# Kernel tuning notes

Hardware: AMD Instinct MI355X
Metric: run time of the kernel (lower is better)

## Reference

```python
import jax, jax.numpy as jnp
import numpy as np

N_NODES = 100000
N_EDGES = 1600000
IN_CH = 64
OUT_CH = 32
HEADS = 4
NEG_SLOPE = 0.2


def setup_inputs() -> dict:
    key = jax.random.key(0)
    k = jax.random.split(key, 6)
    x = jax.random.normal(k[0], (N_NODES, IN_CH), dtype=jnp.float32)
    edge_index = jax.random.randint(k[1], (2, N_EDGES), 0, N_NODES, dtype=jnp.int32)
    W = jax.random.normal(k[2], (IN_CH, HEADS * OUT_CH), dtype=jnp.float32) * 0.1
    att_src = jax.random.normal(k[3], (1, HEADS, OUT_CH), dtype=jnp.float32) * 0.1
    att_dst = jax.random.normal(k[4], (1, HEADS, OUT_CH), dtype=jnp.float32) * 0.1
    bias = jnp.zeros((HEADS * OUT_CH,), dtype=jnp.float32)
    return {"x": x, "edge_index": edge_index, "W": W,
            "att_src": att_src, "att_dst": att_dst, "bias": bias}


def reference(x, edge_index, W, att_src, att_dst, bias):
    N = x.shape[0]
    H, C = att_src.shape[1], att_src.shape[2]
    # GATConv defaults: add self loops
    loop = jnp.arange(N, dtype=edge_index.dtype)
    src = jnp.concatenate([edge_index[0], loop])  # [E+N]
    dst = jnp.concatenate([edge_index[1], loop])  # [E+N]
    # linear transform -> [N, H, C]
    h = (x @ W).reshape(N, H, C)
    # per-node attention halves: [N, H]
    a_src = jnp.sum(h * att_src, axis=-1)
    a_dst = jnp.sum(h * att_dst, axis=-1)
    # edge scores with LeakyReLU: [E+N, H]
    e = jax.nn.leaky_relu(a_src[src] + a_dst[dst], negative_slope=NEG_SLOPE)
    # segment softmax over destination nodes (numerically stable)
    m = jax.ops.segment_max(e, dst, num_segments=N)           # [N, H]
    m = jnp.where(jnp.isfinite(m), m, 0.0)
    ex = jnp.exp(e - m[dst])                                   # [E+N, H]
    denom = jax.ops.segment_sum(ex, dst, num_segments=N)      # [N, H]
    alpha = ex / (denom[dst] + 1e-16)                          # [E+N, H]
    # scatter-aggregate weighted source features -> [N, H, C]
    out = jax.ops.segment_sum(h[src] * alpha[:, :, None], dst, num_segments=N)
    out = out.reshape(N, H * C) + bias
    return jax.nn.log_softmax(out, axis=1)
```

## Files before the change

### kernel.cpp

```cpp
#include <hip/hip_runtime.h>
#include <hip/hip_bf16.h>

#define IN_CH 64
#define HC 128
#define NHEAD 4
#define NEG 0.2f
#define CAPB 32
#define BWID 128
#define NB 782
#define CAP2 2560
#define CH1 4096
#define VPT 8

typedef short s16x8 __attribute__((ext_vector_type(8)));
typedef float f32x4 __attribute__((ext_vector_type(4)));

__device__ __forceinline__ float leaky(float v) { return fmaxf(v, NEG * v); }
__device__ __forceinline__ unsigned short f2bf(float f) {
    unsigned int u = __float_as_uint(f);
    u += 0x7fff + ((u >> 16) & 1);
    return (unsigned short)(u >> 16);
}
__device__ __forceinline__ float4 add4(float4 a, float4 b) {
    return make_float4(a.x + b.x, a.y + b.y, a.z + b.z, a.w + b.w);
}
__device__ __forceinline__ float4 leaky4(float4 v) {
    return make_float4(leaky(v.x), leaky(v.y), leaky(v.z), leaky(v.w));
}
__device__ __forceinline__ float4 exp4(float4 v) {
    return make_float4(__expf(v.x), __expf(v.y), __expf(v.z), __expf(v.w));
}
__device__ __forceinline__ float comp4(float4 v, int i) {
    float r = v.x;
    r = (i == 1) ? v.y : r;
    r = (i == 2) ? v.z : r;
    r = (i == 3) ? v.w : r;
    return r;
}

#define ACC8(al, hv)                                                  \
    do {                                                              \
        acc[0] = fmaf((al), __uint_as_float((hv).x << 16), acc[0]);   \
        acc[1] = fmaf((al), __uint_as_float((hv).x & 0xffff0000u), acc[1]); \
        acc[2] = fmaf((al), __uint_as_float((hv).y << 16), acc[2]);   \
        acc[3] = fmaf((al), __uint_as_float((hv).y & 0xffff0000u), acc[3]); \
        acc[4] = fmaf((al), __uint_as_float((hv).z << 16), acc[4]);   \
        acc[5] = fmaf((al), __uint_as_float((hv).z & 0xffff0000u), acc[5]); \
        acc[6] = fmaf((al), __uint_as_float((hv).w << 16), acc[6]);   \
        acc[7] = fmaf((al), __uint_as_float((hv).w & 0xffff0000u), acc[7]); \
    } while (0)

__global__ void __launch_bounds__(512, 4) k_front(
        const float* __restrict__ x, const float* __restrict__ W,
        const float* __restrict__ att_src, const float* __restrict__ att_dst,
        unsigned short* __restrict__ h_bf, float* __restrict__ a_src,
        float* __restrict__ a_dst,
        const int* __restrict__ src, const int* __restrict__ dst,
        int* __restrict__ bcnt, int* __restrict__ pairs,
        int E, int N, int NXB) {
    __shared__ union {
        struct { unsigned short xs[128][72]; unsigned short wt[144][72]; } xf;
        struct { int hist[NB]; int scanbuf[1024]; int startb[NB]; int gbase[NB];
                 int lbuf[CH1]; int gposb[CH1]; } bn;
    } sm;
    const int t = threadIdx.x;
    const int r3 = blockIdx.x % 3;

    if (r3 < 2) {
        const int xb = (blockIdx.x / 3) * 2 + r3;
        if (xb >= NXB) return;
        const int rowbase_blk = xb * 128;

        for (int idx = t; idx < (IN_CH * HC) / 4; idx += 512) {
            const float4 v = ((const float4*)W)[idx];
            const int k = idx >> 5;
            const int c0 = (idx & 31) * 4;
            sm.xf.wt[c0 + 0][k] = f2bf(v.x);
            sm.xf.wt[c0 + 1][k] = f2bf(v.y);
            sm.xf.wt[c0 + 2][k] = f2bf(v.z);
            sm.xf.wt[c0 + 3][k] = f2bf(v.w);
        }
        for (int idx = t; idx < 16 * 64; idx += 512) {
            const int j = idx >> 6, k = idx & 63;
            float v = 0.f;
            if (j < 8) {
                const int h = j & 3;
                const float* att = (j < 4) ? att_src : att_dst;
#pragma unroll
                for (int c = 0; c < 32; ++c)
                    v += W[k * HC + h * 32 + c] * att[h * 32 + c];
            }
            sm.xf.wt[128 + j][k] = f2bf(v);
        }
        for (int idx = t; idx < (128 * IN_CH) / 4; idx += 512) {
            const int row = idx >> 4;
            const int c0 = (idx & 15) * 4;
            const int grow = min(rowbase_blk + row, N - 1);
            const float4 v = ((const float4*)(x + (size_t)grow * IN_CH))[idx & 15];
            const unsigned int p0 = (unsigned int)f2bf(v.x) | ((unsigned int)f2bf(v.y) << 16);
            const unsigned int p1 = (unsigned int)f2bf(v.z) | ((unsigned int)f2bf(v.w) << 16);
            *(uint2*)&sm.xf.xs[row][c0] = make_uint2(p0, p1);
        }
        __syncthreads();

        const int lane = t & 63;
        const int w = t >> 6;
        const int rbase = w * 16;
        const int lr = lane & 15, lq = lane >> 4;

        f32x4 acc[9];
#pragma unroll
        for (int n = 0; n < 9; ++n) acc[n] = (f32x4){0.f, 0.f, 0.f, 0.f};

#pragma unroll
        for (int ks = 0; ks < 2; ++ks) {
            const s16x8 a0 = *(const s16x8*)&sm.xf.xs[rbase + lr][ks * 32 + lq * 8];
#pragma unroll
            for (int n = 0; n < 9; ++n) {
                const s16x8 b = *(const s16x8*)&sm.xf.wt[n * 16 + lr][ks * 32 + lq * 8];
                acc[n] = __builtin_amdgcn_mfma_f32_16x16x32_bf16(a0, b, acc[n], 0, 0, 0);
            }
        }

#pragma unroll
        for (int j = 0; j < 4; ++j) {
            const int grow = rowbase_blk + rbase + lq * 4 + j;
            if (grow >= N) continue;
#pragma unroll
            for (int n = 0; n < 8; ++n)
                h_bf[(size_t)grow * HC + n * 16 + lr] = f2bf(acc[n][j]);
            const float av = acc[8][j];
            if (lr < 4) a_src[grow * NHEAD + lr] = av;
            else if (lr < 8) a_dst[grow * NHEAD + (lr - 4)] = av;
        }
    } else {
        const int bb = blockIdx.x / 3;
        const int base = bb * CH1;
        const int cnt = min(CH1, E - base);

        for (int i = t; i < NB; i += 512) sm.bn.hist[i] = 0;
        __syncthreads();

        int pk[VPT]; int rb[VPT];
#pragma unroll
        for (int k = 0; k < VPT; ++k) {
            const int idx = base + k * 512 + t;
            if (idx < E) {
                const int s = src[idx], d = dst[idx];
                const int b = d >> 7;
                const int dl = d & 127;
                pk[k] = (dl << 17) | s;
                const int rank = atomicAdd(&sm.bn.hist[b], 1);
                rb[k] = (b << 16) | rank;
            } else {
                pk[k] = 0; rb[k] = -1;
            }
        }
        __syncthreads();

        sm.bn.scanbuf[t] = (t < NB) ? sm.bn.hist[t] : 0;
        sm.bn.scanbuf[t + 512] = (t + 512 < NB) ? sm.bn.hist[t + 512] : 0;
        __syncthreads();
        for (int off = 1; off < 1024; off <<= 1) {
            const int a0 = (t >= off) ? sm.bn.scanbuf[t - off] : 0;
            const int a1 = (t + 512 >= off) ? sm.bn.scanbuf[t + 512 - off] : 0;
            __syncthreads();
            sm.bn.scanbuf[t] += a0;
            sm.bn.scanbuf[t + 512] += a1;
            __syncthreads();
        }
        for (int i = t; i < NB; i += 512) {
            const int h = sm.bn.hist[i];
            sm.bn.startb[i] = sm.bn.scanbuf[i] - h;
            sm.bn.gbase[i] = (h > 0) ? atomicAdd(&bcnt[i * 16], h) : 0;
        }
        __syncthreads();

#pragma unroll
        for (int k = 0; k < VPT; ++k) {
            if (rb[k] >= 0) {
                const int b = rb[k] >> 16;
                const int rank = rb[k] & 0xffff;
                const int lpos = sm.bn.startb[b] + rank;
                const int gp = sm.bn.gbase[b] + rank;
                sm.bn.lbuf[lpos] = pk[k];
                sm.bn.gposb[lpos] = (gp < CAP2) ? (b * CAP2 + gp) : -1;
            }
        }
        __syncthreads();

        for (int i = t; i < cnt; i += 512) {
            const int g = sm.bn.gposb[i];
            if (g >= 0) pairs[g] = sm.bn.lbuf[i];
        }
    }
}

__global__ void __launch_bounds__(256) k_fill(
        const int* __restrict__ bcnt, const int* __restrict__ pairs,
        int* __restrict__ srcbuf, int* __restrict__ rowstart,
        int* __restrict__ deg, int N) {
    const int b = blockIdx.x;
    const int t = threadIdx.x;
    __shared__ int scnt[BWID];
    __shared__ int cur[BWID];
    __shared__ int scan2[256];
    __shared__ int slist[CAP2];
    __shared__ int sbase_s;

    int part = 0;
    for (int i = t; i < b; i += 256) part += min(bcnt[i * 16], CAP2);
    scan2[t] = part; __syncthreads();
    for (int off = 128; off > 0; off >>= 1) {
        if (t < off) scan2[t] += scan2[t + off];
        __syncthreads();
    }
    if (t == 0) sbase_s = scan2[0];
    if (t < BWID) scnt[t] = 0;
    __syncthreads();

    const int mc = min(bcnt[b * 16], CAP2);
    const int pb = b * CAP2;

    for (int i = t; i < mc; i += 256)
        atomicAdd(&scnt[pairs[pb + i] >> 17], 1);
    __syncthreads();

    if (t < BWID) scan2[t] = scnt[t];
    __syncthreads();
    for (int off = 1; off < BWID; off <<= 1) {
        const int add = (t >= off && t < BWID) ? scan2[t - off] : 0;
        __syncthreads();
        if (t < BWID) scan2[t] += add;
        __syncthreads();
    }
    if (t < BWID) {
        const int ex = scan2[t] - scnt[t];
        cur[t] = ex;
        const int n = b * BWID + t;
        if (n < N) {
            rowstart[n] = sbase_s + ex;
            deg[n] = scnt[t];
        }
    }
    __syncthreads();

    for (int i = t; i < mc; i += 256) {
        const int e = pairs[pb + i];
        const int p = atomicAdd(&cur[e >> 17], 1);
        slist[p] = e & 0x1ffff;
    }
    __syncthreads();

    for (int i = t; i < mc; i += 256) srcbuf[sbase_s + i] = slist[i];
}

__global__ void __launch_bounds__(256) k_node(
        const int* __restrict__ deg_, const int* __restrict__ rowstart,
        const int* __restrict__ srcbuf,
        const float* __restrict__ a_src, const float* __restrict__ a_dst,
        const unsigned short* __restrict__ h_bf, const float* __restrict__ bias,
        float* __restrict__ out, int N) {
    const int slot = threadIdx.x >> 4;
    const int l = threadIdx.x & 15;
    int n = blockIdx.x * 16 + slot;
    n = min(n, N - 1);
    const int deg = deg_[n];
    const int start = rowstart[n];
    const int dcap = min(deg, CAPB);

    __shared__ float s_ex[16][CAPB + 1][NHEAD];
    __shared__ int   s_src[16][CAPB + 1];

    const float4 ad4  = *(const float4*)(a_dst + n * NHEAD);
    const float4 asn4 = *(const float4*)(a_src + n * NHEAD);

    float4 sum4 = make_float4(0.f, 0.f, 0.f, 0.f);
    for (int j = l; j < dcap; j += 16) {
        const int s = srcbuf[start + j];
        s_src[slot][j] = s;
        const float4 a = *(const float4*)(a_src + s * NHEAD);
        const float4 e4 = exp4(leaky4(add4(a, ad4)));
        *(float4*)&s_ex[slot][j][0] = e4;
        sum4 = add4(sum4, e4);
    }
    for (int j = CAPB + l; j < deg; j += 16) {
        const int s = srcbuf[start + j];
        const float4 a = *(const float4*)(a_src + s * NHEAD);
        sum4 = add4(sum4, exp4(leaky4(add4(a, ad4))));
    }
#pragma unroll
    for (int off = 1; off < 16; off <<= 1) {
        sum4.x += __shfl_xor(sum4.x, off, 64);
        sum4.y += __shfl_xor(sum4.y, off, 64);
        sum4.z += __shfl_xor(sum4.z, off, 64);
        sum4.w += __shfl_xor(sum4.w, off, 64);
    }
    const float4 self4 = exp4(leaky4(add4(asn4, ad4)));
    sum4 = add4(sum4, self4);
    const float4 r4v = make_float4(1.f / (sum4.x + 1e-16f), 1.f / (sum4.y + 1e-16f),
                                   1.f / (sum4.z + 1e-16f), 1.f / (sum4.w + 1e-16f));

    __builtin_amdgcn_wave_barrier();

    const int hd = l >> 2;
    const float rsel = comp4(r4v, hd);
    const float adh  = comp4(ad4, hd);
    float acc[8];
#pragma unroll
    for (int k = 0; k < 8; ++k) acc[k] = 0.f;

    int j = 0;
    for (; j + 2 <= dcap; j += 2) {
        const int s0 = s_src[slot][j];
        const int s1 = s_src[slot][j + 1];
        const uint4 h0 = *(const uint4*)(h_bf + (size_t)s0 * HC + l * 8);
        const uint4 h1 = *(const uint4*)(h_bf + (size_t)s1 * HC + l * 8);
        const float al0 = s_ex[slot][j][hd];
        const float al1 = s_ex[slot][j + 1][hd];
        ACC8(al0, h0);
        ACC8(al1, h1);
    }
    if (j < dcap) {
        const int s0 = s_src[slot][j];
        const uint4 h0 = *(const uint4*)(h_bf + (size_t)s0 * HC + l * 8);
        const float al0 = s_ex[slot][j][hd];
        ACC8(al0, h0);
    }
    for (int jj = CAPB; jj < deg; ++jj) {
        const int s = srcbuf[start + jj];
        const float al = __expf(leaky(a_src[s * NHEAD + hd] + adh));
        const uint4 hv = *(const uint4*)(h_bf + (size_t)s * HC + l * 8);
        ACC8(al, hv);
    }
    {
        const float als = comp4(self4, hd);
        const uint4 hv = *(const uint4*)(h_bf + (size_t)n * HC + l * 8);
        ACC8(als, hv);
    }

    const float4 b0 = *(const float4*)(bias + l * 8);
    const float4 b1 = *(const float4*)(bias + l * 8 + 4);
    acc[0] = acc[0] * rsel + b0.x; acc[1] = acc[1] * rsel + b0.y;
    acc[2] = acc[2] * rsel + b0.z; acc[3] = acc[3] * rsel + b0.w;
    acc[4] = acc[4] * rsel + b1.x; acc[5] = acc[5] * rsel + b1.y;
    acc[6] = acc[6] * rsel + b1.z; acc[7] = acc[7] * rsel + b1.w;

    float mxv = fmaxf(fmaxf(fmaxf(acc[0], acc[1]), fmaxf(acc[2], acc[3])),
                      fmaxf(fmaxf(acc[4], acc[5]), fmaxf(acc[6], acc[7])));
#pragma unroll
    for (int off = 1; off < 16; off <<= 1) mxv = fmaxf(mxv, __shfl_xor(mxv, off, 64));
    float se = 0.f;
#pragma unroll
    for (int k = 0; k < 8; ++k) se += __expf(acc[k] - mxv);
#pragma unroll
    for (int off = 1; off < 16; off <<= 1) se += __shfl_xor(se, off, 64);
    const float lse = mxv + __logf(se);

    float* op = out + (size_t)n * HC + l * 8;
    *(float4*)op = make_float4(acc[0] - lse, acc[1] - lse, acc[2] - lse, acc[3] - lse);
    *(float4*)(op + 4) = make_float4(acc[4] - lse, acc[5] - lse, acc[6] - lse, acc[7] - lse);
}

extern "C" void kernel_launch(void* const* d_in, const int* in_sizes, int n_in,
                              void* d_out, int out_size, void* d_ws, size_t ws_size,
                              hipStream_t stream) {
    const float* x       = (const float*)d_in[0];
    const int*   ei      = (const int*)d_in[1];
    const float* W       = (const float*)d_in[2];
    const float* att_src = (const float*)d_in[3];
    const float* att_dst = (const float*)d_in[4];
    const float* bias    = (const float*)d_in[5];
    float* out = (float*)d_out;

    const int N = in_sizes[0] / IN_CH;
    const int E = in_sizes[1] / 2;
    const int* src = ei;
    const int* dst = ei + E;

    char* wsb = (char*)d_ws;
    unsigned short* h_bf = (unsigned short*)wsb;    wsb += (size_t)N * HC * 2;
    float* a_src  = (float*)wsb;                    wsb += (size_t)N * NHEAD * 4;
    float* a_dst  = (float*)wsb;                    wsb += (size_t)N * NHEAD * 4;
    int*   bcnt   = (int*)wsb;                      wsb += (size_t)NB * 16 * 4;
    int*   pairs  = (int*)wsb;                      wsb += (size_t)NB * CAP2 * 4;
    int*   srcbuf = (int*)wsb;                      wsb += (size_t)E * 4;
    int*   rowstart = (int*)wsb;                    wsb += (size_t)N * 4;
    int*   deg    = (int*)wsb;                      wsb += (size_t)N * 4;

    const int NXB = (N + 127) / 128;
    const int NBB = (E + CH1 - 1) / CH1;

    hipMemsetAsync(bcnt, 0, (size_t)NB * 16 * 4, stream);

    k_front<<<NBB * 3, 512, 0, stream>>>(x, W, att_src, att_dst,
                                         h_bf, a_src, a_dst,
                                         src, dst, bcnt, pairs, E, N, NXB);
    k_fill<<<NB, 256, 0, stream>>>(bcnt, pairs, srcbuf, rowstart, deg, N);
    k_node<<<(N + 15) / 16, 256, 0, stream>>>(deg, rowstart, srcbuf,
                                              a_src, a_dst,
                                              (const unsigned short*)h_bf, bias, out, N);
}
```

Baseline: 211.1 us.

## Fuse bucket CSR fill into node aggregation kernel using shared-memory edge lists

```diff
diff --git a/kernel.cpp b/kernel.cpp
--- a/kernel.cpp
+++ b/kernel.cpp
@@ -50,7 +50,7 @@
         acc[7] = fmaf((al), __uint_as_float((hv).w & 0xffff0000u), acc[7]); \
     } while (0)
 
-__global__ void __launch_bounds__(512, 4) k_front(
+__global__ void __launch_bounds__(512, 2) k_front(
         const float* __restrict__ x, const float* __restrict__ W,
         const float* __restrict__ att_src, const float* __restrict__ att_dst,
         unsigned short* __restrict__ h_bf, float* __restrict__ a_src,
@@ -196,55 +196,41 @@
     }
 }
 
-__global__ void __launch_bounds__(256) k_fill(
+__global__ void __launch_bounds__(256) k_node(
         const int* __restrict__ bcnt, const int* __restrict__ pairs,
-        int* __restrict__ srcbuf, int* __restrict__ rowstart,
-        int* __restrict__ deg, int N) {
+        const float* __restrict__ a_src, const float* __restrict__ a_dst,
+        const unsigned short* __restrict__ h_bf, const float* __restrict__ bias,
+        float* __restrict__ out, int N) {
     const int b = blockIdx.x;
     const int t = threadIdx.x;
-    __shared__ int scnt[BWID];
-    __shared__ int cur[BWID];
-    __shared__ int scan2[256];
-    __shared__ int slist[CAP2];
-    __shared__ int sbase_s;
-
-    int part = 0;
-    for (int i = t; i < b; i += 256) part += min(bcnt[i * 16], CAP2);
-    scan2[t] = part; __syncthreads();
-    for (int off = 128; off > 0; off >>= 1) {
-        if (t < off) scan2[t] += scan2[t + off];
-        __syncthreads();
-    }
-    if (t == 0) sbase_s = scan2[0];
-    if (t < BWID) scnt[t] = 0;
-    __syncthreads();
+    __shared__ int   slist[CAP2];
+    __shared__ int   srow[BWID];
+    __shared__ int   sdeg[BWID];
+    __shared__ int   cur[BWID];
+    __shared__ int   scanb[BWID];
+    __shared__ float s_ex[16][CAPB + 1][NHEAD];
 
     const int mc = min(bcnt[b * 16], CAP2);
     const int pb = b * CAP2;
 
+    if (t < BWID) sdeg[t] = 0;
+    __syncthreads();
     for (int i = t; i < mc; i += 256)
-        atomicAdd(&scnt[pairs[pb + i] >> 17], 1);
-    __syncthreads();
-
-    if (t < BWID) scan2[t] = scnt[t];
+        atomicAdd(&sdeg[pairs[pb + i] >> 17], 1);
+    __syncthreads();
+    if (t < BWID) scanb[t] = sdeg[t];
     __syncthreads();
     for (int off = 1; off < BWID; off <<= 1) {
-        const int add = (t >= off && t < BWID) ? scan2[t - off] : 0;
-        __syncthreads();
-        if (t < BWID) scan2[t] += add;
+        const int add = (t < BWID && t >= off) ? scanb[t - off] : 0;
+        __syncthreads();
+        if (t < BWID) scanb[t] += add;
         __syncthreads();
     }
     if (t < BWID) {
-        const int ex = scan2[t] - scnt[t];
-        cur[t] = ex;
-        const int n = b * BWID + t;
-        if (n < N) {
-            rowstart[n] = sbase_s + ex;
-            deg[n] = scnt[t];
-        }
-    }
-    __syncthreads();
-
+        srow[t] = scanb[t] - sdeg[t];
+        cur[t] = scanb[t] - sdeg[t];
+    }
+    __syncthreads();
     for (int i = t; i < mc; i += 256) {
         const int e = pairs[pb + i];
         const int p = atomicAdd(&cur[e >> 17], 1);
@@ -252,114 +238,113 @@
     }
     __syncthreads();
 
-    for (int i = t; i < mc; i += 256) srcbuf[sbase_s + i] = slist[i];
-}
-
-__global__ void __launch_bounds__(256) k_node(
-        const int* __restrict__ deg_, const int* __restrict__ rowstart,
-        const int* __restrict__ srcbuf,
-        const float* __restrict__ a_src, const float* __restrict__ a_dst,
-        const unsigned short* __restrict__ h_bf, const float* __restrict__ bias,
-        float* __restrict__ out, int N) {
-    const int slot = threadIdx.x >> 4;
-    const int l = threadIdx.x & 15;
-    int n = blockIdx.x * 16 + slot;
-    n = min(n, N - 1);
-    const int deg = deg_[n];
-    const int start = rowstart[n];
-    const int dcap = min(deg, CAPB);
-
-    __shared__ float s_ex[16][CAPB + 1][NHEAD];
-    __shared__ int   s_src[16][CAPB + 1];
-
-    const float4 ad4  = *(const float4*)(a_dst + n * NHEAD);
-    const float4 asn4 = *(const float4*)(a_src + n * NHEAD);
-
-    float4 sum4 = make_float4(0.f, 0.f, 0.f, 0.f);
-    for (int j = l; j < dcap; j += 16) {
-        const int s = srcbuf[start + j];
-        s_src[slot][j] = s;
-        const float4 a = *(const float4*)(a_src + s * NHEAD);
-        const float4 e4 = exp4(leaky4(add4(a, ad4)));
-        *(float4*)&s_ex[slot][j][0] = e4;
-        sum4 = add4(sum4, e4);
-    }
-    for (int j = CAPB + l; j < deg; j += 16) {
-        const int s = srcbuf[start + j];
-        const float4 a = *(const float4*)(a_src + s * NHEAD);
-        sum4 = add4(sum4, exp4(leaky4(add4(a, ad4))));
-    }
-#pragma unroll
-    for (int off = 1; off < 16; off <<= 1) {
-        sum4.x += __shfl_xor(sum4.x, off, 64);
-        sum4.y += __shfl_xor(sum4.y, off, 64);
-        sum4.z += __shfl_xor(sum4.z, off, 64);
-        sum4.w += __shfl_xor(sum4.w, off, 64);
-    }
-    const float4 self4 = exp4(leaky4(add4(asn4, ad4)));
-    sum4 = add4(sum4, self4);
-    const float4 r4v = make_float4(1.f / (sum4.x + 1e-16f), 1.f / (sum4.y + 1e-16f),
-                                   1.f / (sum4.z + 1e-16f), 1.f / (sum4.w + 1e-16f));
-
-    __builtin_amdgcn_wave_barrier();
-
+    const int slot = t >> 4;
+    const int l = t & 15;
     const int hd = l >> 2;
-    const float rsel = comp4(r4v, hd);
-    const float adh  = comp4(ad4, hd);
-    float acc[8];
-#pragma unroll
-    for (int k = 0; k < 8; ++k) acc[k] = 0.f;
-
-    int j = 0;
-    for (; j + 2 <= dcap; j += 2) {
-        const int s0 = s_src[slot][j];
-        const int s1 = s_src[slot][j + 1];
-        const uint4 h0 = *(const uint4*)(h_bf + (size_t)s0 * HC + l * 8);
-        const uint4 h1 = *(const uint4*)(h_bf + (size_t)s1 * HC + l * 8);
-        const float al0 = s_ex[slot][j][hd];
-        const float al1 = s_ex[slot][j + 1][hd];
-        ACC8(al0, h0);
-        ACC8(al1, h1);
-    }
-    if (j < dcap) {
-        const int s0 = s_src[slot][j];
-        const uint4 h0 = *(const uint4*)(h_bf + (size_t)s0 * HC + l * 8);
-        const float al0 = s_ex[slot][j][hd];
-        ACC8(al0, h0);
-    }
-    for (int jj = CAPB; jj < deg; ++jj) {
-        const int s = srcbuf[start + jj];
-        const float al = __expf(leaky(a_src[s * NHEAD + hd] + adh));
-        const uint4 hv = *(const uint4*)(h_bf + (size_t)s * HC + l * 8);
-        ACC8(al, hv);
-    }
-    {
-        const float als = comp4(self4, hd);
-        const uint4 hv = *(const uint4*)(h_bf + (size_t)n * HC + l * 8);
-        ACC8(als, hv);
-    }
-
-    const float4 b0 = *(const float4*)(bias + l * 8);
-    const float4 b1 = *(const float4*)(bias + l * 8 + 4);
-    acc[0] = acc[0] * rsel + b0.x; acc[1] = acc[1] * rsel + b0.y;
-    acc[2] = acc[2] * rsel + b0.z; acc[3] = acc[3] * rsel + b0.w;
-    acc[4] = acc[4] * rsel + b1.x; acc[5] = acc[5] * rsel + b1.y;
-    acc[6] = acc[6] * rsel + b1.z; acc[7] = acc[7] * rsel + b1.w;
-
-    float mxv = fmaxf(fmaxf(fmaxf(acc[0], acc[1]), fmaxf(acc[2], acc[3])),
-                      fmaxf(fmaxf(acc[4], acc[5]), fmaxf(acc[6], acc[7])));
-#pragma unroll
-    for (int off = 1; off < 16; off <<= 1) mxv = fmaxf(mxv, __shfl_xor(mxv, off, 64));
-    float se = 0.f;
-#pragma unroll
-    for (int k = 0; k < 8; ++k) se += __expf(acc[k] - mxv);
-#pragma unroll
-    for (int off = 1; off < 16; off <<= 1) se += __shfl_xor(se, off, 64);
-    const float lse = mxv + __logf(se);
-
-    float* op = out + (size_t)n * HC + l * 8;
-    *(float4*)op = make_float4(acc[0] - lse, acc[1] - lse, acc[2] - lse, acc[3] - lse);
-    *(float4*)(op + 4) = make_float4(acc[4] - lse, acc[5] - lse, acc[6] - lse, acc[7] - lse);
+
+    for (int ng = 0; ng < 8; ++ng) {
+        int dl = ng * 16 + slot;
+        int n = b * BWID + dl;
+        if (n >= N) { n = N - 1; dl = (N - 1) & (BWID - 1); }
+        const int deg = sdeg[dl];
+        const int rs = srow[dl];
+        const int dcap = min(deg, CAPB);
+
+        const float4 ad4  = *(const float4*)(a_dst + n * NHEAD);
+        const float4 asn4 = *(const float4*)(a_src + n * NHEAD);
+
+        float4 sum4 = make_float4(0.f, 0.f, 0.f, 0.f);
+        for (int j = l; j < dcap; j += 16) {
+            const int s = slist[rs + j];
+            const float4 a = *(const float4*)(a_src + s * NHEAD);
+            const float4 e4 = exp4(leaky4(add4(a, ad4)));
+            *(float4*)&s_ex[slot][j][0] = e4;
+            sum4 = add4(sum4, e4);
+        }
+        for (int j = CAPB + l; j < deg; j += 16) {
+            const int s = slist[rs + j];
+            const float4 a = *(const float4*)(a_src + s * NHEAD);
+            sum4 = add4(sum4, exp4(leaky4(add4(a, ad4))));
+        }
+#pragma unroll
+        for (int off = 1; off < 16; off <<= 1) {
+            sum4.x += __shfl_xor(sum4.x, off, 64);
+            sum4.y += __shfl_xor(sum4.y, off, 64);
+            sum4.z += __shfl_xor(sum4.z, off, 64);
+            sum4.w += __shfl_xor(sum4.w, off, 64);
+        }
+        const float4 self4 = exp4(leaky4(add4(asn4, ad4)));
+        sum4 = add4(sum4, self4);
+        const float4 r4v = make_float4(1.f / (sum4.x + 1e-16f), 1.f / (sum4.y + 1e-16f),
+                                       1.f / (sum4.z + 1e-16f), 1.f / (sum4.w + 1e-16f));
+
+        __builtin_amdgcn_wave_barrier();
+
+        const float rsel = comp4(r4v, hd);
+        const float adh  = comp4(ad4, hd);
+        float acc[8];
+#pragma unroll
+        for (int k = 0; k < 8; ++k) acc[k] = 0.f;
+
+        int j = 0;
+        for (; j + 4 <= dcap; j += 4) {
+            const int s0 = slist[rs + j];
+            const int s1 = slist[rs + j + 1];
+            const int s2 = slist[rs + j + 2];
+            const int s3 = slist[rs + j + 3];
+            const uint4 h0 = *(const uint4*)(h_bf + (size_t)s0 * HC + l * 8);
+            const uint4 h1 = *(const uint4*)(h_bf + (size_t)s1 * HC + l * 8);
+            const uint4 h2 = *(const uint4*)(h_bf + (size_t)s2 * HC + l * 8);
+            const uint4 h3 = *(const uint4*)(h_bf + (size_t)s3 * HC + l * 8);
+            const float al0 = s_ex[slot][j][hd];
+            const float al1 = s_ex[slot][j + 1][hd];
+            const float al2 = s_ex[slot][j + 2][hd];
+            const float al3 = s_ex[slot][j + 3][hd];
+            ACC8(al0, h0);
+            ACC8(al1, h1);
+            ACC8(al2, h2);
+            ACC8(al3, h3);
+        }
+        for (; j < dcap; ++j) {
+            const int s0 = slist[rs + j];
+            const uint4 h0 = *(const uint4*)(h_bf + (size_t)s0 * HC + l * 8);
+            const float al0 = s_ex[slot][j][hd];
+            ACC8(al0, h0);
+        }
+        for (int jj = CAPB; jj < deg; ++jj) {
+            const int s = slist[rs + jj];
+            const float al = __expf(leaky(a_src[s * NHEAD + hd] + adh));
+            const uint4 hv = *(const uint4*)(h_bf + (size_t)s * HC + l * 8);
+            ACC8(al, hv);
+        }
+        {
+            const float als = comp4(self4, hd);
+            const uint4 hv = *(const uint4*)(h_bf + (size_t)n * HC + l * 8);
+            ACC8(als, hv);
+        }
+
+        const float4 b0 = *(const float4*)(bias + l * 8);
+        const float4 b1 = *(const float4*)(bias + l * 8 + 4);
+        acc[0] = acc[0] * rsel + b0.x; acc[1] = acc[1] * rsel + b0.y;
+        acc[2] = acc[2] * rsel + b0.z; acc[3] = acc[3] * rsel + b0.w;
+        acc[4] = acc[4] * rsel + b1.x; acc[5] = acc[5] * rsel + b1.y;
+        acc[6] = acc[6] * rsel + b1.z; acc[7] = acc[7] * rsel + b1.w;
+
+        float mxv = fmaxf(fmaxf(fmaxf(acc[0], acc[1]), fmaxf(acc[2], acc[3])),
+                          fmaxf(fmaxf(acc[4], acc[5]), fmaxf(acc[6], acc[7])));
+#pragma unroll
+        for (int off = 1; off < 16; off <<= 1) mxv = fmaxf(mxv, __shfl_xor(mxv, off, 64));
+        float se = 0.f;
+#pragma unroll
+        for (int k = 0; k < 8; ++k) se += __expf(acc[k] - mxv);
+#pragma unroll
+        for (int off = 1; off < 16; off <<= 1) se += __shfl_xor(se, off, 64);
+        const float lse = mxv + __logf(se);
+
+        float* op = out + (size_t)n * HC + l * 8;
+        *(float4*)op = make_float4(acc[0] - lse, acc[1] - lse, acc[2] - lse, acc[3] - lse);
+        *(float4*)(op + 4) = make_float4(acc[4] - lse, acc[5] - lse, acc[6] - lse, acc[7] - lse);
+    }
 }
 
 extern "C" void kernel_launch(void* const* d_in, const int* in_sizes, int n_in,
@@ -384,9 +369,6 @@
     float* a_dst  = (float*)wsb;                    wsb += (size_t)N * NHEAD * 4;
     int*   bcnt   = (int*)wsb;                      wsb += (size_t)NB * 16 * 4;
     int*   pairs  = (int*)wsb;                      wsb += (size_t)NB * CAP2 * 4;
-    int*   srcbuf = (int*)wsb;                      wsb += (size_t)E * 4;
-    int*   rowstart = (int*)wsb;                    wsb += (size_t)N * 4;
-    int*   deg    = (int*)wsb;                      wsb += (size_t)N * 4;
 
     const int NXB = (N + 127) / 128;
     const int NBB = (E + CH1 - 1) / CH1;
@@ -396,8 +378,6 @@
     k_front<<<NBB * 3, 512, 0, stream>>>(x, W, att_src, att_dst,
                                          h_bf, a_src, a_dst,
                                          src, dst, bcnt, pairs, E, N, NXB);
-    k_fill<<<NB, 256, 0, stream>>>(bcnt, pairs, srcbuf, rowstart, deg, N);
-    k_node<<<(N + 15) / 16, 256, 0, stream>>>(deg, rowstart, srcbuf,
-                                              a_src, a_dst,
-                                              (const unsigned short*)h_bf, bias, out, N);
-}
+    k_node<<<NB, 256, 0, stream>>>(bcnt, pairs, a_src, a_dst,
+                                   (const unsigned short*)h_bf, bias, out, N);
+}
```

New measurement: 210.3 us. No clear change (-0.3%).

## Precompute bf16 weight tile once in a prep kernel and unroll gather by eight

Applied to the files above, without the earlier changes.

```diff
diff --git a/kernel.cpp b/kernel.cpp
--- a/kernel.cpp
+++ b/kernel.cpp
@@ -50,9 +50,31 @@
         acc[7] = fmaf((al), __uint_as_float((hv).w & 0xffff0000u), acc[7]); \
     } while (0)
 
-__global__ void __launch_bounds__(512, 4) k_front(
-        const float* __restrict__ x, const float* __restrict__ W,
-        const float* __restrict__ att_src, const float* __restrict__ att_dst,
+__global__ void __launch_bounds__(256) k_prep(
+        const float* __restrict__ W, const float* __restrict__ att_src,
+        const float* __restrict__ att_dst, unsigned short* __restrict__ wtp,
+        int* __restrict__ bcnt) {
+    const int t = threadIdx.x;
+    for (int i = t; i < NB * 16; i += 256) bcnt[i] = 0;
+    for (int idx = t; idx < 144 * 64; idx += 256) {
+        const int c = idx >> 6, k = idx & 63;
+        float v = 0.f;
+        if (c < HC) v = W[k * HC + c];
+        else if (c < HC + 8) {
+            const int j = c - HC, h = j & 3;
+            const float* att = (j < 4) ? att_src : att_dst;
+#pragma unroll
+            for (int cc = 0; cc < 32; ++cc)
+                v += W[k * HC + h * 32 + cc] * att[h * 32 + cc];
+        }
+        wtp[c * 72 + k] = f2bf(v);
+    }
+    for (int idx = t; idx < 144 * 8; idx += 256)
+        wtp[(idx >> 3) * 72 + 64 + (idx & 7)] = 0;
+}
+
+__global__ void __launch_bounds__(512, 2) k_front(
+        const float* __restrict__ x, const unsigned short* __restrict__ wtp,
         unsigned short* __restrict__ h_bf, float* __restrict__ a_src,
         float* __restrict__ a_dst,
         const int* __restrict__ src, const int* __restrict__ dst,
@@ -71,27 +93,8 @@
         if (xb >= NXB) return;
         const int rowbase_blk = xb * 128;
 
-        for (int idx = t; idx < (IN_CH * HC) / 4; idx += 512) {
-            const float4 v = ((const float4*)W)[idx];
-            const int k = idx >> 5;
-            const int c0 = (idx & 31) * 4;
-            sm.xf.wt[c0 + 0][k] = f2bf(v.x);
-            sm.xf.wt[c0 + 1][k] = f2bf(v.y);
-            sm.xf.wt[c0 + 2][k] = f2bf(v.z);
-            sm.xf.wt[c0 + 3][k] = f2bf(v.w);
-        }
-        for (int idx = t; idx < 16 * 64; idx += 512) {
-            const int j = idx >> 6, k = idx & 63;
-            float v = 0.f;
-            if (j < 8) {
-                const int h = j & 3;
-                const float* att = (j < 4) ? att_src : att_dst;
-#pragma unroll
-                for (int c = 0; c < 32; ++c)
-                    v += W[k * HC + h * 32 + c] * att[h * 32 + c];
-            }
-            sm.xf.wt[128 + j][k] = f2bf(v);
-        }
+        for (int idx = t; idx < 1296; idx += 512)
+            ((uint4*)sm.xf.wt)[idx] = ((const uint4*)wtp)[idx];
         for (int idx = t; idx < (128 * IN_CH) / 4; idx += 512) {
             const int row = idx >> 4;
             const int c0 = (idx & 15) * 4;
@@ -311,6 +314,34 @@
     for (int k = 0; k < 8; ++k) acc[k] = 0.f;
 
     int j = 0;
+    for (; j + 8 <= dcap; j += 8) {
+        const int s0 = s_src[slot][j];
+        const int s1 = s_src[slot][j + 1];
+        const int s2 = s_src[slot][j + 2];
+        const int s3 = s_src[slot][j + 3];
+        const int s4 = s_src[slot][j + 4];
+        const int s5 = s_src[slot][j + 5];
+        const int s6 = s_src[slot][j + 6];
+        const int s7 = s_src[slot][j + 7];
+        const uint4 h0 = *(const uint4*)(h_bf + (size_t)s0 * HC + l * 8);
+        const uint4 h1 = *(const uint4*)(h_bf + (size_t)s1 * HC + l * 8);
+        const uint4 h2 = *(const uint4*)(h_bf + (size_t)s2 * HC + l * 8);
+        const uint4 h3 = *(const uint4*)(h_bf + (size_t)s3 * HC + l * 8);
+        const uint4 h4 = *(const uint4*)(h_bf + (size_t)s4 * HC + l * 8);
+        const uint4 h5 = *(const uint4*)(h_bf + (size_t)s5 * HC + l * 8);
+        const uint4 h6 = *(const uint4*)(h_bf + (size_t)s6 * HC + l * 8);
+        const uint4 h7 = *(const uint4*)(h_bf + (size_t)s7 * HC + l * 8);
+        const float al0 = s_ex[slot][j][hd];
+        const float al1 = s_ex[slot][j + 1][hd];
+        const float al2 = s_ex[slot][j + 2][hd];
+        const float al3 = s_ex[slot][j + 3][hd];
+        const float al4 = s_ex[slot][j + 4][hd];
+        const float al5 = s_ex[slot][j + 5][hd];
+        const float al6 = s_ex[slot][j + 6][hd];
+        const float al7 = s_ex[slot][j + 7][hd];
+        ACC8(al0, h0); ACC8(al1, h1); ACC8(al2, h2); ACC8(al3, h3);
+        ACC8(al4, h4); ACC8(al5, h5); ACC8(al6, h6); ACC8(al7, h7);
+    }
     for (; j + 2 <= dcap; j += 2) {
         const int s0 = s_src[slot][j];
         const int s1 = s_src[slot][j + 1];
@@ -387,14 +418,13 @@
     int*   srcbuf = (int*)wsb;                      wsb += (size_t)E * 4;
     int*   rowstart = (int*)wsb;                    wsb += (size_t)N * 4;
     int*   deg    = (int*)wsb;                      wsb += (size_t)N * 4;
+    unsigned short* wtp = (unsigned short*)wsb;     wsb += 144 * 72 * 2;
 
     const int NXB = (N + 127) / 128;
     const int NBB = (E + CH1 - 1) / CH1;
 
-    hipMemsetAsync(bcnt, 0, (size_t)NB * 16 * 4, stream);
-
-    k_front<<<NBB * 3, 512, 0, stream>>>(x, W, att_src, att_dst,
-                                         h_bf, a_src, a_dst,
+    k_prep<<<1, 256, 0, stream>>>(W, att_src, att_dst, wtp, bcnt);
+    k_front<<<NBB * 3, 512, 0, stream>>>(x, wtp, h_bf, a_src, a_dst,
                                          src, dst, bcnt, pairs, E, N, NXB);
     k_fill<<<NB, 256, 0, stream>>>(bcnt, pairs, srcbuf, rowstart, deg, N);
     k_node<<<(N + 15) / 16, 256, 0, stream>>>(deg, rowstart, srcbuf,
```

Result: slower. 219.4 us (+3.9%).
